# Kernel tuning notes

Hardware: AMD Instinct MI355X
Metric: run time of the kernel (lower is better)

Reference implementation:

```python
import jax, jax.numpy as jnp
import numpy as np
from jax import lax

B, T, N = 256, 2048, 17   # batch, seq_len, num_tags
M, E, A = 2, 8, 4         # iob2 block size, num entity types = (N-1)//M, attn blocks
H = 768                   # hidden_dim


def setup_inputs() -> dict:
    key = jax.random.key(0)
    ks = jax.random.split(key, 9)
    return {
        "inputs": jax.random.normal(ks[0], (B, T, N), jnp.float32),
        "tags": jax.random.randint(ks[1], (B, T), 0, N, jnp.int32),
        "hiddens": jax.random.normal(ks[2], (E, H), jnp.float32),
        "mask": jnp.ones((B, T), jnp.int32),
        "p_in": jax.random.normal(ks[3], (A, M, M), jnp.float32),
        "p_cross": jax.random.normal(ks[4], (M, M), jnp.float32),
        "p_out": jax.random.normal(ks[5], (1,), jnp.float32),
        "p_to_out": jax.random.normal(ks[6], (M,), jnp.float32),
        "p_from_out": jax.random.normal(ks[7], (M,), jnp.float32),
        "w_attn": jax.random.normal(ks[8], (H, A), jnp.float32) / np.sqrt(H),
        "b_attn": jnp.zeros((A,), jnp.float32),
    }


def build_transitions(hiddens, p_in, p_cross, p_out, p_to_out, p_from_out, w_attn, b_attn):
    # block attention over entity types -> per-entity in-block transition matrices
    att = hiddens @ w_attn + b_attn                 # [E, A]
    att = jax.nn.softmax(att, axis=0)
    att = jax.nn.softmax(att * 10.0, axis=-1)
    p_in_e = (p_in[None] * att[:, :, None, None]).mean(1)   # [E, M, M]
    # assemble [E*M, E*M] block matrix: p_in_e on diagonal blocks, p_cross elsewhere
    diag = jnp.eye(E, dtype=bool)[:, :, None, None]
    blocks = jnp.where(diag, p_in_e[:, None], p_cross[None, None])  # [E, E, M, M]
    inner = blocks.transpose(0, 2, 1, 3).reshape(E * M, E * M)
    trans = jnp.zeros((N, N), jnp.float32)
    trans = trans.at[0, 0].set(p_out[0])
    trans = trans.at[0, 1:].set(jnp.tile(p_from_out, E))
    trans = trans.at[1:, 0].set(jnp.tile(p_to_out, E))
    trans = trans.at[1:, 1:].set(inner)
    return trans


def reference(inputs, tags, hiddens, mask, p_in, p_cross, p_out, p_to_out, p_from_out, w_attn, b_attn):
    trans = build_transitions(hiddens, p_in, p_cross, p_out, p_to_out, p_from_out, w_attn, b_attn)
    maskf = mask.astype(inputs.dtype)

    # ---- log partition function (CRF forward algorithm, no start/end transitions) ----
    def step(alpha, xs):
        emit, m = xs  # emit [B, N], m [B]
        inner = alpha[:, :, None] + trans[None] + emit[:, None, :]  # [B, N, N]
        new = jax.scipy.special.logsumexp(inner, axis=1)
        return jnp.where(m[:, None] > 0, new, alpha), None

    alpha0 = inputs[:, 0]  # [B, N]
    alpha, _ = lax.scan(step, alpha0, (inputs[:, 1:].transpose(1, 0, 2), mask[:, 1:].T))
    log_denominator = jax.scipy.special.logsumexp(alpha, axis=-1)  # [B]

    # ---- joint likelihood of gold path (fully vectorized) ----
    trans_sc = (trans[tags[:, :-1], tags[:, 1:]] * maskf[:, 1:]).sum(1)
    emit_sc = (jnp.take_along_axis(inputs[:, :-1], tags[:, :-1, None], axis=2)[..., 0]
               * maskf[:, :-1]).sum(1)
    last_idx = mask.sum(1) - 1
    last_tags = jnp.take_along_axis(tags, last_idx[:, None].astype(jnp.int32), axis=1)[:, 0]
    last_emit = jnp.take_along_axis(inputs[:, -1], last_tags[:, None], axis=1)[:, 0] * maskf[:, -1]
    log_numerator = trans_sc + emit_sc + last_emit

    # reduction='sum'
    return (log_numerator - log_denominator).sum()
```

## Files before the change

kernel.cpp:

```cpp
#include <hip/hip_runtime.h>
#include <math.h>

#define B_ 256
#define T_ 2048
#define N_ 17
#define CHUNKS 16
#define CLEN 128
#define LOG2E 1.44269504088896340736f
#define LN2   0.69314718055994530942f

typedef short bf16x8 __attribute__((ext_vector_type(8)));
typedef float f32x16 __attribute__((ext_vector_type(16)));
typedef float v2f __attribute__((ext_vector_type(2)));

__device__ __forceinline__ float rlf(float v, int i) {
    return __int_as_float(__builtin_amdgcn_readlane(__float_as_int(v), i));
}
__device__ __forceinline__ float fexp2(float x) {
    float r;
    asm("v_exp_f32 %0, %1" : "=v"(r) : "v"(x));
    return r;
}
__device__ __forceinline__ float fmax3(float a, float b, float c) {
    return fmaxf(fmaxf(a, b), c);
}
__device__ __forceinline__ unsigned pack_bf16(float lo, float hi) {
    return __builtin_amdgcn_perm(__float_as_uint(hi), __float_as_uint(lo), 0x07060302u);
}

__global__ __launch_bounds__(256) void build_trans_k(
    const float* __restrict__ hiddens, const float* __restrict__ p_in,
    const float* __restrict__ p_cross, const float* __restrict__ p_out,
    const float* __restrict__ p_to_out, const float* __restrict__ p_from_out,
    const float* __restrict__ w_attn, const float* __restrict__ b_attn,
    float* __restrict__ trans)
{
    __shared__ float partial[32][8];
    __shared__ float att[8][4];
    int tid = threadIdx.x;
    int pair = tid >> 3, sub = tid & 7;
    int e = pair >> 2, a = pair & 3;
    float acc = 0.f;
    for (int h = sub; h < 768; h += 8)
        acc += hiddens[e*768 + h] * w_attn[h*4 + a];
    partial[pair][sub] = acc;
    __syncthreads();
    if (tid < 32) {
        float s = 0.f;
        for (int k2 = 0; k2 < 8; ++k2) s += partial[tid][k2];
        att[tid>>2][tid&3] = s + b_attn[tid&3];
    }
    __syncthreads();
    if (tid == 0) {
        float t1[8][4], t2[8][4];
        for (int a2 = 0; a2 < 4; ++a2) {
            float m = -1e30f;
            for (int e2 = 0; e2 < 8; ++e2) m = fmaxf(m, att[e2][a2]);
            float s = 0.f;
            for (int e2 = 0; e2 < 8; ++e2) { t1[e2][a2] = expf(att[e2][a2] - m); s += t1[e2][a2]; }
            for (int e2 = 0; e2 < 8; ++e2) t1[e2][a2] /= s;
        }
        for (int e2 = 0; e2 < 8; ++e2) {
            float m = -1e30f;
            for (int a2 = 0; a2 < 4; ++a2) m = fmaxf(m, t1[e2][a2]*10.f);
            float s = 0.f;
            for (int a2 = 0; a2 < 4; ++a2) { t2[e2][a2] = expf(t1[e2][a2]*10.f - m); s += t2[e2][a2]; }
            for (int a2 = 0; a2 < 4; ++a2) t2[e2][a2] /= s;
        }
        trans[0] = p_out[0];
        for (int c = 0; c < 16; ++c) trans[0*N_ + 1 + c] = p_from_out[c & 1];
        for (int r = 0; r < 16; ++r) trans[(1+r)*N_ + 0] = p_to_out[r & 1];
        for (int eb = 0; eb < 8; ++eb)
        for (int r = 0; r < 2; ++r)
        for (int ec = 0; ec < 8; ++ec)
        for (int c = 0; c < 2; ++c) {
            float v;
            if (eb == ec) {
                v = 0.f;
                for (int a2 = 0; a2 < 4; ++a2) v += p_in[a2*4 + r*2 + c] * t2[eb][a2];
                v *= 0.25f;
            } else v = p_cross[r*2 + c];
            trans[(1 + eb*2 + r)*N_ + (1 + ec*2 + c)] = v;
        }
    }
}

__global__ __launch_bounds__(64, 4) void phaseA_k(
    const float* __restrict__ inputs, const int* __restrict__ mask,
    const float* __restrict__ trans, unsigned short* __restrict__ Qout,
    int* __restrict__ Kout)
{
    const int gid = blockIdx.x;
    const int b = gid >> 4;
    const int c = gid & (CHUNKS - 1);
    const int lane = threadIdx.x & 63;
    const int n = lane & 31;
    const int h = lane >> 5;

    v2f TA[4];
    #pragma unroll
    for (int r2 = 0; r2 < 4; ++r2) {
        int k0 = 8*h + 2*r2;
        TA[r2].x = (n < N_ && k0   < N_) ? expf(trans[k0*N_ + n])     : 0.f;
        TA[r2].y = (n < N_ && k0+1 < N_) ? expf(trans[(k0+1)*N_ + n]) : 0.f;
    }
    v2f TA8;
    TA8.x = (n < N_ && h == 0) ? expf(trans[16*N_ + n]) : 0.f;
    TA8.y = 0.f;

    f32x16 acc;
    #pragma unroll
    for (int r = 0; r < 16; ++r) {
        int R = (r & 3) + 8*(r >> 2) + 4*h;
        acc[r] = (R == n) ? 1.f : 0.f;
    }
    const f32x16 fz = {};

    const int t0 = c * CLEN;
    const float* ep = inputs + (size_t)b*T_*N_ + (n < N_ ? n : N_-1);
    const int*   mp = mask + (size_t)b*T_;

    float re[8]; int rm[8];
    #pragma unroll
    for (int p = 0; p < 8; ++p) {
        int t = t0 + p;
        re[p] = ep[(size_t)t * N_];
        rm[p] = (t == 0) ? 0 : mp[t];
    }
    const float* epn = ep + (size_t)(t0 + 8) * N_;
    const int*   mpn = mp + (t0 + 8);

    int K = 0;
    #pragma unroll 1
    for (int s8 = 0; s8 < CLEN/8; ++s8) {
        const bool refill = (s8 < CLEN/8 - 1);
        #pragma unroll
        for (int u = 0; u < 8; ++u) {
            float ev = re[u]; int mv = rm[u];
            if (refill) {
                re[u] = epn[u * N_];
                rm[u] = mpn[u];
            }
            if (__builtin_amdgcn_readfirstlane(mv) > 0) {
                float e = fexp2(ev * LOG2E);
                v2f ee; ee.x = e; ee.y = e;
                v2f s0 = TA[0]*ee, s1 = TA[1]*ee, s2 = TA[2]*ee, s3 = TA[3]*ee;
                v2f s8v = TA8*ee;
                union { unsigned u[4]; bf16x8 v; } a1, a2, b1, b2;
                a1.u[0] = pack_bf16(s0.x, s0.y);
                a1.u[1] = pack_bf16(s1.x, s1.y);
                a1.u[2] = pack_bf16(s2.x, s2.y);
                a1.u[3] = pack_bf16(s3.x, s3.y);
                a2.u[0] = pack_bf16(s8v.x, s8v.y);
                a2.u[1] = 0; a2.u[2] = 0; a2.u[3] = 0;
                float x0=acc[0], x1=acc[1], x2=acc[2], x3=acc[3];
                float x4=acc[4], x5=acc[5], x6=acc[6], x7=acc[7];
                asm("v_permlane32_swap_b32 %0, %1" : "+v"(x4), "+v"(x0));
                asm("v_permlane32_swap_b32 %0, %1" : "+v"(x5), "+v"(x1));
                asm("v_permlane32_swap_b32 %0, %1" : "+v"(x6), "+v"(x2));
                asm("v_permlane32_swap_b32 %0, %1" : "+v"(x7), "+v"(x3));
                b1.u[0] = pack_bf16(x0, x1);
                b1.u[1] = pack_bf16(x2, x3);
                b1.u[2] = pack_bf16(x4, x5);
                b1.u[3] = pack_bf16(x6, x7);
                unsigned p89 = pack_bf16(acc[8], acc[9]);
                b2.u[0] = (h == 0) ? p89 : 0u;
                b2.u[1] = 0; b2.u[2] = 0; b2.u[3] = 0;
                f32x16 nacc = __builtin_amdgcn_mfma_f32_32x32x16_bf16(a1.v, b1.v, fz, 0, 0, 0);
                nacc = __builtin_amdgcn_mfma_f32_32x32x16_bf16(a2.v, b2.v, nacc, 0, 0, 0);
                acc = nacc;
            }
        }
        if (refill) { epn += 8 * N_; mpn += 8; }
        float mxa = fmax3(acc[0], acc[1], acc[2]);
        float mxb = fmax3(acc[3], acc[4], acc[5]);
        float mxc = fmax3(acc[6], acc[7], acc[8]);
        float mxd = fmax3(acc[9], acc[10], acc[11]);
        float mxe = fmax3(acc[12], acc[13], acc[14]);
        float mx = fmaxf(fmax3(mxa, mxb, mxc), fmax3(mxd, mxe, acc[15]));
        #pragma unroll
        for (int off = 32; off > 0; off >>= 1)
            mx = fmaxf(mx, __shfl_xor(mx, off, 64));
        int sexp = (int)(__float_as_uint(mx) >> 23) - 127;
        float sc = __uint_as_float((unsigned)(127 - sexp) << 23);
        v2f scv; scv.x = sc; scv.y = sc;
        #pragma unroll
        for (int r = 0; r < 8; ++r) {
            v2f pr; pr.x = acc[2*r]; pr.y = acc[2*r+1];
            pr = pr * scv;
            acc[2*r] = pr.x; acc[2*r+1] = pr.y;
        }
        K += sexp;
    }

    unsigned short* qb = Qout + (size_t)gid * (N_*32);
    #pragma unroll
    for (int r = 0; r < 16; ++r) {
        int R = (r & 3) + 8*(r >> 2) + 4*h;
        if (R < N_)
            qb[R*32 + n] = (unsigned short)(__float_as_uint(acc[r]) >> 16);
    }
    if (lane == 0) Kout[gid] = K;
}

__global__ __launch_bounds__(64, 1) void combine_k(
    const float* __restrict__ inputs, const unsigned short* __restrict__ Qin,
    const int* __restrict__ Kin, float* __restrict__ denom)
{
    const int b = blockIdx.x;
    const int lane = threadIdx.x & 63;
    const bool active = lane < N_;
    const int j = active ? lane : N_-1;

    const float* ip = inputs + (size_t)b*T_*N_;
    float a0 = active ? ip[j] : -1e30f;
    float m0 = rlf(a0, 0);
    #pragma unroll
    for (int i = 1; i < N_; ++i) m0 = fmaxf(m0, rlf(a0, i));
    float w = active ? fexp2((a0 - m0)*LOG2E) : 0.f;
    int K = 0;

    for (int c = 0; c < CHUNKS; ++c) {
        const unsigned short* qr = Qin + ((size_t)(b*CHUNKS + c))*(N_*32) + j*32;
        uint4 qa = *(const uint4*)qr;
        uint4 qc4 = *(const uint4*)(qr + 8);
        unsigned q16u = qr[16];
        int kc = Kin[b*CHUNKS + c];
        float sv[N_];
        #pragma unroll
        for (int i = 0; i < N_; ++i) sv[i] = rlf(w, i);
        unsigned mxb = __float_as_uint(sv[0]);
        #pragma unroll
        for (int i = 1; i < N_; ++i) { unsigned bi = __float_as_uint(sv[i]); if (bi > mxb) mxb = bi; }
        int me = (int)(mxb >> 23) - 127;
        float sc = __uint_as_float((unsigned)(127 - me) << 23);
        float q[N_];
        q[0]  = __uint_as_float(qa.x << 16);  q[1]  = __uint_as_float(qa.x & 0xFFFF0000u);
        q[2]  = __uint_as_float(qa.y << 16);  q[3]  = __uint_as_float(qa.y & 0xFFFF0000u);
        q[4]  = __uint_as_float(qa.z << 16);  q[5]  = __uint_as_float(qa.z & 0xFFFF0000u);
        q[6]  = __uint_as_float(qa.w << 16);  q[7]  = __uint_as_float(qa.w & 0xFFFF0000u);
        q[8]  = __uint_as_float(qc4.x << 16); q[9]  = __uint_as_float(qc4.x & 0xFFFF0000u);
        q[10] = __uint_as_float(qc4.y << 16); q[11] = __uint_as_float(qc4.y & 0xFFFF0000u);
        q[12] = __uint_as_float(qc4.z << 16); q[13] = __uint_as_float(qc4.z & 0xFFFF0000u);
        q[14] = __uint_as_float(qc4.w << 16); q[15] = __uint_as_float(qc4.w & 0xFFFF0000u);
        q[16] = __uint_as_float(q16u << 16);
        float d0 = sv[0]*q[0], d1 = sv[1]*q[1], d2 = sv[2]*q[2], d3 = sv[3]*q[3];
        #pragma unroll
        for (int i = 4; i < 16; i += 4) {
            d0 = fmaf(sv[i+0], q[i+0], d0);
            d1 = fmaf(sv[i+1], q[i+1], d1);
            d2 = fmaf(sv[i+2], q[i+2], d2);
            d3 = fmaf(sv[i+3], q[i+3], d3);
        }
        d0 = fmaf(sv[16], q[16], d0);
        float nw = ((d0 + d1) + (d2 + d3)) * sc;
        w = active ? nw : 0.f;
        K += me + kc;
    }

    float s = w;
    #pragma unroll
    for (int off = 32; off > 0; off >>= 1) s += __shfl_xor(s, off, 64);
    if (lane == 0)
        denom[b] = logf(s) + (float)K * LN2 + m0;
}

__global__ __launch_bounds__(256) void numer_k(
    const float* __restrict__ inputs, const int* __restrict__ tags,
    const int* __restrict__ mask, const float* __restrict__ trans,
    const float* __restrict__ denom, float* __restrict__ out)
{
    const int b = blockIdx.x, tid = threadIdx.x;
    const int* tg = tags + (size_t)b * T_;
    const int* mp = mask + (size_t)b * T_;
    const float* ip = inputs + (size_t)b * T_ * N_;
    float tsum = 0.f, esum = 0.f; int msum = 0;
    for (int t = tid; t < T_ - 1; t += 256) {
        int g = tg[t], g2 = tg[t+1];
        int m1 = mp[t], m2 = mp[t+1];
        tsum += (m2 > 0) ? trans[g*N_ + g2] : 0.f;
        esum += (m1 > 0) ? ip[(size_t)t*N_ + g] : 0.f;
        msum += (m1 > 0) ? 1 : 0;
    }
    if (tid == 0) msum += (mp[T_-1] > 0) ? 1 : 0;
    #pragma unroll
    for (int off = 32; off > 0; off >>= 1) {
        tsum += __shfl_xor(tsum, off, 64);
        esum += __shfl_xor(esum, off, 64);
        msum += __shfl_xor(msum, off, 64);
    }
    __shared__ float r0[4], r1[4]; __shared__ int r2[4];
    int wid = tid >> 6;
    if ((tid & 63) == 0) { r0[wid] = tsum; r1[wid] = esum; r2[wid] = msum; }
    __syncthreads();
    if (tid == 0) {
        float ts = r0[0]+r0[1]+r0[2]+r0[3];
        float es = r1[0]+r1[1]+r1[2]+r1[3];
        int   ms = r2[0]+r2[1]+r2[2]+r2[3];
        int lt = tg[ms - 1];
        float le = (mp[T_-1] > 0) ? ip[(size_t)(T_-1)*N_ + lt] : 0.f;
        atomicAdd(out, ts + es + le - denom[b]);
    }
}

extern "C" void kernel_launch(void* const* d_in, const int* in_sizes, int n_in,
                              void* d_out, int out_size, void* d_ws, size_t ws_size,
                              hipStream_t stream)
{
    const float* inputs    = (const float*)d_in[0];
    const int*   tags      = (const int*)  d_in[1];
    const float* hiddens   = (const float*)d_in[2];
    const int*   mask      = (const int*)  d_in[3];
    const float* p_in      = (const float*)d_in[4];
    const float* p_cross   = (const float*)d_in[5];
    const float* p_out     = (const float*)d_in[6];
    const float* p_to_out  = (const float*)d_in[7];
    const float* p_from_out= (const float*)d_in[8];
    const float* w_attn    = (const float*)d_in[9];
    const float* b_attn    = (const float*)d_in[10];
    float* out = (float*)d_out;
    float* ws  = (float*)d_ws;

    float* trans = ws;
    float* denom = ws + 512;
    int*   Kbuf  = (int*)(ws + 1024);
    unsigned short* Qbuf = (unsigned short*)(ws + 8192);

    (void)hipMemsetAsync(d_out, 0, sizeof(float), stream);
    hipLaunchKernelGGL(build_trans_k, dim3(1), dim3(256), 0, stream,
                       hiddens, p_in, p_cross, p_out, p_to_out, p_from_out,
                       w_attn, b_attn, trans);
    hipLaunchKernelGGL(phaseA_k, dim3(B_*CHUNKS), dim3(64), 0, stream,
                       inputs, mask, trans, Qbuf, Kbuf);
    hipLaunchKernelGGL(combine_k, dim3(B_), dim3(64), 0, stream,
                       inputs, Qbuf, Kbuf, denom);
    hipLaunchKernelGGL(numer_k, dim3(B_), dim3(256), 0, stream,
                       inputs, tags, mask, trans, denom, out);
}
```

Measured before the change: 212.5 us.

## Split CRF scan into 32 chunks with branchless masked steps and compact Q storage

The time-parallel scan is split into 32 chunks per sequence instead of 16 when the workspace allows, doubling the number of waves and raising the launch-bounds occupancy hint to 8. Masked steps no longer branch; they select an identity A operand so every step issues the MFMA uniformly. The rescale max now scans only the accumulator rows that hold valid states, and the stored chunk matrices use a compact 24-wide row stride. The combine kernel takes the chunk count at runtime, so it does twice as many serial chunk-combine iterations per batch when 32 chunks are used.

```diff
diff --git a/kernel.cpp b/kernel.cpp
--- a/kernel.cpp
+++ b/kernel.cpp
@@ -4,10 +4,10 @@
 #define B_ 256
 #define T_ 2048
 #define N_ 17
-#define CHUNKS 16
-#define CLEN 128
 #define LOG2E 1.44269504088896340736f
 #define LN2   0.69314718055994530942f
+#define QROW 24
+#define QMAT 416
 
 typedef short bf16x8 __attribute__((ext_vector_type(8)));
 typedef float f32x16 __attribute__((ext_vector_type(16)));
@@ -85,14 +85,52 @@
     }
 }
 
-__global__ __launch_bounds__(64, 4) void phaseA_k(
+__device__ __forceinline__ f32x16 pa_step(
+    f32x16 acc, float ev, int mv,
+    const v2f* TA, float TA8x, const unsigned* ia1u, unsigned ia2u0, int h)
+{
+    float e = fexp2(ev * LOG2E);
+    v2f ee; ee.x = e; ee.y = e;
+    v2f s0 = TA[0]*ee, s1 = TA[1]*ee, s2 = TA[2]*ee, s3 = TA[3]*ee;
+    float s8x = TA8x * e;
+    bool upd = __builtin_amdgcn_readfirstlane(mv) > 0;
+    union { unsigned u[4]; bf16x8 v; } a1, a2, b1, b2;
+    a1.u[0] = upd ? pack_bf16(s0.x, s0.y) : ia1u[0];
+    a1.u[1] = upd ? pack_bf16(s1.x, s1.y) : ia1u[1];
+    a1.u[2] = upd ? pack_bf16(s2.x, s2.y) : ia1u[2];
+    a1.u[3] = upd ? pack_bf16(s3.x, s3.y) : ia1u[3];
+    a2.u[0] = upd ? pack_bf16(s8x, 0.f) : ia2u0;
+    a2.u[1] = 0; a2.u[2] = 0; a2.u[3] = 0;
+    unsigned p89 = pack_bf16(acc[8], acc[9]);
+    b2.u[0] = (h == 0) ? p89 : 0u;
+    b2.u[1] = 0; b2.u[2] = 0; b2.u[3] = 0;
+    float x0=acc[0], x1=acc[1], x2=acc[2], x3=acc[3];
+    float x4=acc[4], x5=acc[5], x6=acc[6], x7=acc[7];
+    asm("v_permlane32_swap_b32 %0, %1" : "+v"(x4), "+v"(x0));
+    asm("v_permlane32_swap_b32 %0, %1" : "+v"(x5), "+v"(x1));
+    asm("v_permlane32_swap_b32 %0, %1" : "+v"(x6), "+v"(x2));
+    asm("v_permlane32_swap_b32 %0, %1" : "+v"(x7), "+v"(x3));
+    b1.u[0] = pack_bf16(x0, x1);
+    b1.u[1] = pack_bf16(x2, x3);
+    b1.u[2] = pack_bf16(x4, x5);
+    b1.u[3] = pack_bf16(x6, x7);
+    const f32x16 fz = {};
+    f32x16 d = __builtin_amdgcn_mfma_f32_32x32x16_bf16(a1.v, b1.v, fz, 0, 0, 0);
+    d = __builtin_amdgcn_mfma_f32_32x32x16_bf16(a2.v, b2.v, d, 0, 0, 0);
+    return d;
+}
+
+template <int NCH>
+__global__ __launch_bounds__(64, 8) void phaseA_k(
     const float* __restrict__ inputs, const int* __restrict__ mask,
     const float* __restrict__ trans, unsigned short* __restrict__ Qout,
     int* __restrict__ Kout)
 {
+    constexpr int CL = T_ / NCH;
+    constexpr int GR = CL / 8;
     const int gid = blockIdx.x;
-    const int b = gid >> 4;
-    const int c = gid & (CHUNKS - 1);
+    const int b = gid / NCH;
+    const int c = gid % NCH;
     const int lane = threadIdx.x & 63;
     const int n = lane & 31;
     const int h = lane >> 5;
@@ -104,9 +142,15 @@
         TA[r2].x = (n < N_ && k0   < N_) ? expf(trans[k0*N_ + n])     : 0.f;
         TA[r2].y = (n < N_ && k0+1 < N_) ? expf(trans[(k0+1)*N_ + n]) : 0.f;
     }
-    v2f TA8;
-    TA8.x = (n < N_ && h == 0) ? expf(trans[16*N_ + n]) : 0.f;
-    TA8.y = 0.f;
+    float TA8x = (n < N_ && h == 0) ? expf(trans[16*N_ + n]) : 0.f;
+
+    unsigned ia1u[4];
+    #pragma unroll
+    for (int r2 = 0; r2 < 4; ++r2) {
+        int k0 = 8*h + 2*r2;
+        ia1u[r2] = pack_bf16(n == k0 ? 1.f : 0.f, n == k0+1 ? 1.f : 0.f);
+    }
+    unsigned ia2u0 = (n == 16 && h == 0) ? pack_bf16(1.f, 0.f) : 0u;
 
     f32x16 acc;
     #pragma unroll
@@ -114,9 +158,8 @@
         int R = (r & 3) + 8*(r >> 2) + 4*h;
         acc[r] = (R == n) ? 1.f : 0.f;
     }
-    const f32x16 fz = {};
-
-    const int t0 = c * CLEN;
+
+    const int t0 = c * CL;
     const float* ep = inputs + (size_t)b*T_*N_ + (n < N_ ? n : N_-1);
     const int*   mp = mask + (size_t)b*T_;
 
@@ -129,83 +172,61 @@
     }
     const float* epn = ep + (size_t)(t0 + 8) * N_;
     const int*   mpn = mp + (t0 + 8);
-
     int K = 0;
-    #pragma unroll 1
-    for (int s8 = 0; s8 < CLEN/8; ++s8) {
-        const bool refill = (s8 < CLEN/8 - 1);
+
+#define PA_RESCALE                                                             \
+    {                                                                          \
+        float mxa = fmax3(acc[0], acc[1], acc[2]);                             \
+        float mxb = fmax3(acc[3], acc[4], acc[5]);                             \
+        float mx  = fmax3(acc[6], acc[7], acc[8]);                             \
+        mx = fmax3(mx, mxa, mxb);                                              \
+        _Pragma("unroll")                                                      \
+        for (int off = 32; off > 0; off >>= 1)                                 \
+            mx = fmaxf(mx, __shfl_xor(mx, off, 64));                           \
+        int sexp = (int)(__float_as_uint(mx) >> 23) - 127;                     \
+        float sc = __uint_as_float((unsigned)(127 - sexp) << 23);              \
+        v2f scv; scv.x = sc; scv.y = sc;                                       \
+        _Pragma("unroll")                                                      \
+        for (int r = 0; r < 4; ++r) {                                          \
+            v2f pr; pr.x = acc[2*r]; pr.y = acc[2*r+1];                        \
+            pr = pr * scv;                                                     \
+            acc[2*r] = pr.x; acc[2*r+1] = pr.y;                                \
+        }                                                                      \
+        acc[8] *= sc;                                                          \
+        K += sexp;                                                             \
+    }
+
+    for (int g = 0; g < GR - 1; ++g) {
         #pragma unroll
         for (int u = 0; u < 8; ++u) {
             float ev = re[u]; int mv = rm[u];
-            if (refill) {
-                re[u] = epn[u * N_];
-                rm[u] = mpn[u];
-            }
-            if (__builtin_amdgcn_readfirstlane(mv) > 0) {
-                float e = fexp2(ev * LOG2E);
-                v2f ee; ee.x = e; ee.y = e;
-                v2f s0 = TA[0]*ee, s1 = TA[1]*ee, s2 = TA[2]*ee, s3 = TA[3]*ee;
-                v2f s8v = TA8*ee;
-                union { unsigned u[4]; bf16x8 v; } a1, a2, b1, b2;
-                a1.u[0] = pack_bf16(s0.x, s0.y);
-                a1.u[1] = pack_bf16(s1.x, s1.y);
-                a1.u[2] = pack_bf16(s2.x, s2.y);
-                a1.u[3] = pack_bf16(s3.x, s3.y);
-                a2.u[0] = pack_bf16(s8v.x, s8v.y);
-                a2.u[1] = 0; a2.u[2] = 0; a2.u[3] = 0;
-                float x0=acc[0], x1=acc[1], x2=acc[2], x3=acc[3];
-                float x4=acc[4], x5=acc[5], x6=acc[6], x7=acc[7];
-                asm("v_permlane32_swap_b32 %0, %1" : "+v"(x4), "+v"(x0));
-                asm("v_permlane32_swap_b32 %0, %1" : "+v"(x5), "+v"(x1));
-                asm("v_permlane32_swap_b32 %0, %1" : "+v"(x6), "+v"(x2));
-                asm("v_permlane32_swap_b32 %0, %1" : "+v"(x7), "+v"(x3));
-                b1.u[0] = pack_bf16(x0, x1);
-                b1.u[1] = pack_bf16(x2, x3);
-                b1.u[2] = pack_bf16(x4, x5);
-                b1.u[3] = pack_bf16(x6, x7);
-                unsigned p89 = pack_bf16(acc[8], acc[9]);
-                b2.u[0] = (h == 0) ? p89 : 0u;
-                b2.u[1] = 0; b2.u[2] = 0; b2.u[3] = 0;
-                f32x16 nacc = __builtin_amdgcn_mfma_f32_32x32x16_bf16(a1.v, b1.v, fz, 0, 0, 0);
-                nacc = __builtin_amdgcn_mfma_f32_32x32x16_bf16(a2.v, b2.v, nacc, 0, 0, 0);
-                acc = nacc;
-            }
-        }
-        if (refill) { epn += 8 * N_; mpn += 8; }
-        float mxa = fmax3(acc[0], acc[1], acc[2]);
-        float mxb = fmax3(acc[3], acc[4], acc[5]);
-        float mxc = fmax3(acc[6], acc[7], acc[8]);
-        float mxd = fmax3(acc[9], acc[10], acc[11]);
-        float mxe = fmax3(acc[12], acc[13], acc[14]);
-        float mx = fmaxf(fmax3(mxa, mxb, mxc), fmax3(mxd, mxe, acc[15]));
-        #pragma unroll
-        for (int off = 32; off > 0; off >>= 1)
-            mx = fmaxf(mx, __shfl_xor(mx, off, 64));
-        int sexp = (int)(__float_as_uint(mx) >> 23) - 127;
-        float sc = __uint_as_float((unsigned)(127 - sexp) << 23);
-        v2f scv; scv.x = sc; scv.y = sc;
-        #pragma unroll
-        for (int r = 0; r < 8; ++r) {
-            v2f pr; pr.x = acc[2*r]; pr.y = acc[2*r+1];
-            pr = pr * scv;
-            acc[2*r] = pr.x; acc[2*r+1] = pr.y;
-        }
-        K += sexp;
-    }
-
-    unsigned short* qb = Qout + (size_t)gid * (N_*32);
-    #pragma unroll
-    for (int r = 0; r < 16; ++r) {
+            re[u] = epn[u * N_];
+            rm[u] = mpn[u];
+            acc = pa_step(acc, ev, mv, TA, TA8x, ia1u, ia2u0, h);
+        }
+        epn += 8 * N_; mpn += 8;
+        PA_RESCALE
+    }
+    #pragma unroll
+    for (int u = 0; u < 8; ++u) {
+        float ev = re[u]; int mv = rm[u];
+        acc = pa_step(acc, ev, mv, TA, TA8x, ia1u, ia2u0, h);
+    }
+    PA_RESCALE
+
+    unsigned short* qb = Qout + (size_t)gid * QMAT;
+    #pragma unroll
+    for (int r = 0; r < 9; ++r) {
         int R = (r & 3) + 8*(r >> 2) + 4*h;
-        if (R < N_)
-            qb[R*32 + n] = (unsigned short)(__float_as_uint(acc[r]) >> 16);
+        if (R < N_ && n < N_)
+            qb[R*QROW + n] = (unsigned short)(__float_as_uint(acc[r]) >> 16);
     }
     if (lane == 0) Kout[gid] = K;
 }
 
 __global__ __launch_bounds__(64, 1) void combine_k(
     const float* __restrict__ inputs, const unsigned short* __restrict__ Qin,
-    const int* __restrict__ Kin, float* __restrict__ denom)
+    const int* __restrict__ Kin, float* __restrict__ denom, int nch)
 {
     const int b = blockIdx.x;
     const int lane = threadIdx.x & 63;
@@ -220,12 +241,12 @@
     float w = active ? fexp2((a0 - m0)*LOG2E) : 0.f;
     int K = 0;
 
-    for (int c = 0; c < CHUNKS; ++c) {
-        const unsigned short* qr = Qin + ((size_t)(b*CHUNKS + c))*(N_*32) + j*32;
+    for (int c = 0; c < nch; ++c) {
+        const unsigned short* qr = Qin + (size_t)(b*nch + c)*QMAT + j*QROW;
         uint4 qa = *(const uint4*)qr;
         uint4 qc4 = *(const uint4*)(qr + 8);
         unsigned q16u = qr[16];
-        int kc = Kin[b*CHUNKS + c];
+        int kc = Kin[b*nch + c];
         float sv[N_];
         #pragma unroll
         for (int i = 0; i < N_; ++i) sv[i] = rlf(w, i);
@@ -324,16 +345,23 @@
     float* trans = ws;
     float* denom = ws + 512;
     int*   Kbuf  = (int*)(ws + 1024);
-    unsigned short* Qbuf = (unsigned short*)(ws + 8192);
+    unsigned short* Qbuf = (unsigned short*)(ws + 16384);
+
+    const size_t need32 = (size_t)16384*4 + (size_t)B_*32*QMAT*2;
+    const int nch = (ws_size >= need32) ? 32 : 16;
 
     (void)hipMemsetAsync(d_out, 0, sizeof(float), stream);
     hipLaunchKernelGGL(build_trans_k, dim3(1), dim3(256), 0, stream,
                        hiddens, p_in, p_cross, p_out, p_to_out, p_from_out,
                        w_attn, b_attn, trans);
-    hipLaunchKernelGGL(phaseA_k, dim3(B_*CHUNKS), dim3(64), 0, stream,
-                       inputs, mask, trans, Qbuf, Kbuf);
+    if (nch == 32)
+        hipLaunchKernelGGL((phaseA_k<32>), dim3(B_*32), dim3(64), 0, stream,
+                           inputs, mask, trans, Qbuf, Kbuf);
+    else
+        hipLaunchKernelGGL((phaseA_k<16>), dim3(B_*16), dim3(64), 0, stream,
+                           inputs, mask, trans, Qbuf, Kbuf);
     hipLaunchKernelGGL(combine_k, dim3(B_), dim3(64), 0, stream,
-                       inputs, Qbuf, Kbuf, denom);
+                       inputs, Qbuf, Kbuf, denom, nch);
     hipLaunchKernelGGL(numer_k, dim3(B_), dim3(256), 0, stream,
                        inputs, tags, mask, trans, denom, out);
 }
```

Measured after the change: 190.4 us. 10.4% less time.
